# Kernel optimization log

Hardware: AMD Instinct MI355X
Metric: run time of the kernel (lower is better)

The kernel has to match this reference:

```python
import jax, jax.numpy as jnp
from jax import lax
import numpy as np

B, N0 = 4, 4096
NIN, NH, NOUT = 16, 128, 2
DEPTH, K, RADIUS, KNN = 3, 64, 2.0, 3
EPS = 1e-5


def _bn(x, g, b):
    # eval-mode BatchNorm1d with running_mean=0, running_var=1
    return g * x / jnp.sqrt(1.0 + EPS) + b


def _mlp2(h, p):
    # Seq(Lin, ReLU, BN) x 2, as in MLP([d, d, out])
    w1, b1, g1, be1, w2, b2, g2, be2 = p
    h = _bn(jax.nn.relu(h @ w1 + b1), g1, be1)
    return _bn(jax.nn.relu(h @ w2 + b2), g2, be2)


def _fps(pts, m):
    # farthest point sampling, deterministic start at index 0
    n = pts.shape[0]
    def step(carry, _):
        dmin, last = carry
        d = jnp.sum((pts - pts[last]) ** 2, axis=-1)
        dmin = jnp.minimum(dmin, d)
        nxt = jnp.argmax(dmin).astype(jnp.int32)
        return (dmin, nxt), nxt
    _, rest = lax.scan(step, (jnp.full((n,), 1e30, pts.dtype), jnp.int32(0)), None, length=m - 1)
    return jnp.concatenate([jnp.zeros((1,), jnp.int32), rest])


def _sa(xx, pp, m, params):
    # SAModule with PointConv: fps -> radius(K nearest within r) -> gather-MLP-max
    idx = _fps(pp, m)
    q = pp[idx]                                              # [m,3] sampled centers
    d2 = jnp.sum((q[:, None, :] - pp[None, :, :]) ** 2, -1)  # [m,n]
    d2 = jnp.where(d2 <= RADIUS * RADIUS, d2, 1e30)
    neg, nbr = lax.top_k(-d2, K)                             # K nearest inside ball
    valid = neg > -1e29
    h = jnp.concatenate([xx[nbr], pp[nbr] - q[:, None, :]], axis=-1)  # [m,K,C+3]
    h = _mlp2(h, params)
    h = jnp.where(valid[..., None], h, -1e30)
    return jnp.max(h, axis=1), q                             # PointConv max aggr


def _fp(xx, pp, xs, ps, params):
    # FPModule: knn_interpolate (k=3, inverse squared-distance weights) + concat skip + MLP
    d2 = jnp.sum((ps[:, None, :] - pp[None, :, :]) ** 2, -1)  # [n_fine, n_coarse]
    neg, idx = lax.top_k(-d2, KNN)
    w = 1.0 / jnp.maximum(-neg, 1e-16)
    y = jnp.sum(w[..., None] * xx[idx], axis=1) / jnp.sum(w, axis=1, keepdims=True)
    return _mlp2(jnp.concatenate([y, xs], axis=-1), params)


def _forward(x, pos, lin_in_w, lin_in_b,
             sa_w1, sa_b1, sa_g1, sa_be1, sa_w2, sa_b2, sa_g2, sa_be2,
             fp_w1, fp_b1, fp_g1, fp_be1, fp_w2, fp_b2, fp_g2, fp_be2,
             lo_w1, lo_b1, lo_g1, lo_be1, lo_w2, lo_b2, lo_g2, lo_be2):
    xb = jax.nn.relu(x.reshape(B, N0, NIN) @ lin_in_w + lin_in_b)  # lin_in + ReLU
    posb = pos.reshape(B, N0, 3)
    sa = [(xb, posb)]
    n = N0
    for i in range(DEPTH):
        m = n // 2  # ratio = 0.5
        p = (sa_w1[i], sa_b1[i], sa_g1[i], sa_be1[i], sa_w2[i], sa_b2[i], sa_g2[i], sa_be2[i])
        h, q = jax.vmap(lambda a, b: _sa(a, b, m, p))(sa[i][0], sa[i][1])
        sa.append((h, q))
        n = m
    xf, posf = sa[DEPTH]
    for step in range(DEPTH):
        mi = DEPTH - 1 - step
        xs, ps = sa[DEPTH - 1 - step]
        p = (fp_w1[mi], fp_b1[mi], fp_g1[mi], fp_be1[mi], fp_w2[mi], fp_b2[mi], fp_g2[mi], fp_be2[mi])
        xf = jax.vmap(lambda a, b, c, d: _fp(a, b, c, d, p))(xf, posf, xs, ps)
        posf = ps
    out = _mlp2(xf, (lo_w1, lo_b1, lo_g1, lo_be1, lo_w2, lo_b2, lo_g2, lo_be2))
    return out.reshape(B * N0, NOUT)


def setup_inputs() -> dict:
    key = jax.random.key(0)
    ki = iter(jax.random.split(key, 24))
    def nrm(shape, s=0.1):
        return jax.random.normal(next(ki), shape, jnp.float32) * s
    D = NH + 3   # PointConv MLP in-dim
    F = 2 * NH   # FP MLP in-dim (nIn + nSkip)
    return {
        "x": jax.random.normal(next(ki), (B * N0, NIN), jnp.float32),
        "pos": jax.random.uniform(next(ki), (B * N0, 3), jnp.float32) * 16.0,
        "batch": jnp.repeat(jnp.arange(B, dtype=jnp.int32), N0),
        "lin_in_w": nrm((NIN, NH)), "lin_in_b": nrm((NH,)),
        "sa_w1": nrm((DEPTH, D, D)), "sa_b1": nrm((DEPTH, D)),
        "sa_g1": jnp.ones((DEPTH, D)), "sa_be1": jnp.zeros((DEPTH, D)),
        "sa_w2": nrm((DEPTH, D, NH)), "sa_b2": nrm((DEPTH, NH)),
        "sa_g2": jnp.ones((DEPTH, NH)), "sa_be2": jnp.zeros((DEPTH, NH)),
        "fp_w1": nrm((DEPTH, F, F)), "fp_b1": nrm((DEPTH, F)),
        "fp_g1": jnp.ones((DEPTH, F)), "fp_be1": jnp.zeros((DEPTH, F)),
        "fp_w2": nrm((DEPTH, F, NH)), "fp_b2": nrm((DEPTH, NH)),
        "fp_g2": jnp.ones((DEPTH, NH)), "fp_be2": jnp.zeros((DEPTH, NH)),
        "lo_w1": nrm((NH, NH)), "lo_b1": nrm((NH,)),
        "lo_g1": jnp.ones((NH,)), "lo_be1": jnp.zeros((NH,)),
        "lo_w2": nrm((NH, NOUT)), "lo_b2": nrm((NOUT,)),
        "lo_g2": jnp.ones((NOUT,)), "lo_be2": jnp.zeros((NOUT,)),
    }


def reference(x, pos, batch, lin_in_w, lin_in_b,
              sa_w1, sa_b1, sa_g1, sa_be1, sa_w2, sa_b2, sa_g2, sa_be2,
              fp_w1, fp_b1, fp_g1, fp_be1, fp_w2, fp_b2, fp_g2, fp_be2,
              lo_w1, lo_b1, lo_g1, lo_be1, lo_w2, lo_b2, lo_g2, lo_be2):
    return _forward(x, pos, lin_in_w, lin_in_b,
                    sa_w1, sa_b1, sa_g1, sa_be1, sa_w2, sa_b2, sa_g2, sa_be2,
                    fp_w1, fp_b1, fp_g1, fp_be1, fp_w2, fp_b2, fp_g2, fp_be2,
                    lo_w1, lo_b1, lo_g1, lo_be1, lo_w2, lo_b2, lo_g2, lo_be2)
```

## Files before the change

kernel.cpp:

```cpp
#include <hip/hip_runtime.h>
#include <cstddef>


#define EPSF 1e-5f

typedef __attribute__((ext_vector_type(2))) float f32x2;

__device__ __forceinline__ f32x2 f2splat(float s) {
    f32x2 v; v.x = s; v.y = s; return v;
}

__device__ __forceinline__ float d2_rn(float dx, float dy, float dz) {
    return __fadd_rn(__fadd_rn(__fmul_rn(dx, dx), __fmul_rn(dy, dy)), __fmul_rn(dz, dz));
}

template <int CTRL, int RMASK>
__device__ __forceinline__ float dpp_max_f32(float v) {
    int o = __builtin_amdgcn_update_dpp(__float_as_int(v), __float_as_int(v),
                                        CTRL, RMASK, 0xf, false);
    return fmaxf(v, __int_as_float(o));
}

template <int N, int NT>
__device__ void fps_role(const float* __restrict__ pts, float* __restrict__ q,
                         const int m, const int b, char* smem) {
#pragma clang fp contract(off)
    constexpr int PPT = N / NT;
    constexpr int PH = PPT / 2;
    constexpr int NW = NT / 64;
    float* s_px = (float*)smem;
    float* s_py = s_px + N;
    float* s_pz = s_py + N;
    int*   s_qi = (int*)(s_pz + N);
    float2* s_slot = (float2*)(s_qi + N / 2);
    const int t = threadIdx.x;
    const int wave = t >> 6, lane = t & 63;
    const int base = t * PPT;
    const float* P = pts + (size_t)b * N * 3;
    asm volatile("s_setprio 3");
    f32x2 rx[PH], ry[PH], rz[PH], dmin[PH];
#pragma unroll
    for (int j = 0; j < PH; ++j) {
        int i = base + 2 * j;
        float x0 = P[i * 3 + 0], y0 = P[i * 3 + 1], z0 = P[i * 3 + 2];
        float x1 = P[i * 3 + 3], y1 = P[i * 3 + 4], z1 = P[i * 3 + 5];
        rx[j].x = x0; rx[j].y = x1;
        ry[j].x = y0; ry[j].y = y1;
        rz[j].x = z0; rz[j].y = z1;
        dmin[j] = f2splat(1e30f);
        s_px[i] = x0; s_px[i + 1] = x1;
        s_py[i] = y0; s_py[i + 1] = y1;
        s_pz[i] = z0; s_pz[i + 1] = z1;
    }
    float lx = P[0], ly = P[1], lz = P[2];
    if (t == 0) s_qi[0] = 0;

    for (int step = 1; step < m; ++step) {
        float bv = -1.0f; int bj = 0;
        const f32x2 lxv = f2splat(lx), lyv = f2splat(ly), lzv = f2splat(lz);
#pragma unroll
        for (int j = 0; j < PH; ++j) {
            f32x2 dx = rx[j] - lxv;
            f32x2 dy = ry[j] - lyv;
            f32x2 dz = rz[j] - lzv;
            f32x2 d = dx * dx + dy * dy + dz * dz;
            float m0 = fminf(dmin[j].x, d.x);
            float m1 = fminf(dmin[j].y, d.y);
            dmin[j].x = m0; dmin[j].y = m1;
            if (m0 > bv) { bv = m0; bj = 2 * j; }
            if (m1 > bv) { bv = m1; bj = 2 * j + 1; }
        }
        const int bidx = base + bj;

        float v = bv;
        v = dpp_max_f32<0x111, 0xf>(v);
        v = dpp_max_f32<0x112, 0xf>(v);
        v = dpp_max_f32<0x114, 0xf>(v);
        v = dpp_max_f32<0x118, 0xf>(v);
        v = dpp_max_f32<0x142, 0xa>(v);
        v = dpp_max_f32<0x143, 0xc>(v);
        const float mv = __int_as_float(__builtin_amdgcn_readlane(__float_as_int(v), 63));
        unsigned long long mb = __ballot(bv == mv);
        const int wl = __ffsll((long long)mb) - 1;
        const int wbi = __builtin_amdgcn_readlane(bidx, wl);

        const int p = step & 1;
        if (lane == 0) s_slot[p * NW + wave] = make_float2(mv, __int_as_float(wbi));
        __syncthreads();

        float2 sl = s_slot[p * NW + (lane & (NW - 1))];
        float gvt = sl.x;
        gvt = dpp_max_f32<0x111, 0xf>(gvt);
        gvt = dpp_max_f32<0x112, 0xf>(gvt);
        if (NW == 8) gvt = dpp_max_f32<0x114, 0xf>(gvt);
        const float gm = __int_as_float(
            __builtin_amdgcn_readlane(__float_as_int(gvt), NW - 1));
        unsigned long long gb = __ballot((lane < NW) && (sl.x == gm));
        const int gl = __ffsll((long long)gb) - 1;
        const int gi = __builtin_amdgcn_readlane(__float_as_int(sl.y), gl);

        lx = s_px[gi]; ly = s_py[gi]; lz = s_pz[gi];
        if (t == 0) s_qi[step] = gi;
    }
    __syncthreads();
    for (int e = t; e < m; e += NT) {
        int gi = s_qi[e];
        size_t o = ((size_t)b * m + e) * 3;
        q[o] = s_px[gi]; q[o + 1] = s_py[gi]; q[o + 2] = s_pz[gi];
    }
}

__device__ void lin_role(const float* __restrict__ x, const float* __restrict__ w,
                         const float* __restrict__ bias, float* __restrict__ xb,
                         const int blk) {
    const int t = threadIdx.x;
    const int row = blk * 2 + (t >> 7);
    const int col = t & 127;
    float acc = bias[col];
#pragma unroll
    for (int k = 0; k < 16; ++k) acc = fmaf(x[row * 16 + k], w[k * 128 + col], acc);
    xb[row * 128 + col] = fmaxf(acc, 0.0f);
}

template <int CHUNK, int WACT>
__device__ void nbr_role(const float* __restrict__ pts, const float* __restrict__ q,
                         int2* __restrict__ pairs, unsigned* __restrict__ counter,
                         const int n, const int m, const int blk, char* smem) {
    const int w = threadIdx.x >> 6, lane = threadIdx.x & 63;
    if (w >= WACT) return;
    float* D = (float*)smem + w * CHUNK * 64;
    const int c = blk * WACT + w;
    const int b = c / m;
    const float* P = pts + (size_t)b * n * 3;
    const float qx = q[(size_t)c * 3 + 0];
    const float qy = q[(size_t)c * 3 + 1];
    const float qz = q[(size_t)c * 3 + 2];
    for (int s = 0; s < CHUNK; ++s) {
        int i = s * 64 + lane;
        float d2 = d2_rn(P[i * 3] - qx, P[i * 3 + 1] - qy, P[i * 3 + 2] - qz);
        D[i] = (d2 <= 4.0f) ? d2 : 1e30f;
    }
    int my_g = -1;
    int cnt = 0;
    for (int round = 0; round < 64; ++round) {
        float bv = 3e38f;
        int bi = 0x7fffffff;
        for (int s = 0; s < CHUNK; ++s) {
            int i = s * 64 + lane;
            float v = D[i];
            if (v < bv) { bv = v; bi = i; }
        }
#pragma unroll
        for (int off = 32; off >= 1; off >>= 1) {
            float ov = __shfl_xor(bv, off, 64);
            int   oi = __shfl_xor(bi, off, 64);
            if (ov < bv || (ov == bv && oi < bi)) { bv = ov; bi = oi; }
        }
        if (bv > 1e29f) break;
        if (round == lane) my_g = bi;
        if (lane == (bi & 63)) D[bi] = 3e38f;
        ++cnt;
    }
    unsigned base = 0;
    if (lane == 0) base = atomicAdd(counter, (unsigned)cnt);
    base = (unsigned)__shfl((int)base, 0, 64);
    if (lane < cnt) pairs[base + lane] = make_int2(c, my_g);
}

typedef float Row132[132];
__device__ void sa_body(const float* __restrict__ xx, const float* __restrict__ pts,
    const float* __restrict__ q, const int2* __restrict__ pairs,
    const unsigned* __restrict__ vcount,
    const float* __restrict__ wp1, const float* __restrict__ b1,
    const float* __restrict__ g1, const float* __restrict__ be1,
    const float* __restrict__ wp2, const float* __restrict__ b2,
    const float* __restrict__ g2, const float* __restrict__ be2,
    float* __restrict__ hout, const int lm, const int ln, const int blk, char* smem) {
    Row132* shA = (Row132*)smem;
    int* sh_c = (int*)(smem + 33792);
    int* sh_g = sh_c + 64;
    const int t = threadIdx.x;
    const int V = (int)*vcount;
    const int r0 = blk * 64;
    if (r0 >= V) return;
    if (t < 64) {
        int r = r0 + t;
        if (r < V) { int2 p = pairs[r]; sh_c[t] = p.x; sh_g[t] = p.y; }
        else { sh_c[t] = -1; sh_g[t] = 0; }
    }
    __syncthreads();

    for (int e = t; e < 64 * 33; e += 256) {
        int row = e / 33, cid = e - row * 33;
        int c = sh_c[row];
        float4 v = make_float4(0.f, 0.f, 0.f, 0.f);
        if (c >= 0) {
            int g = sh_g[row];
            int b = c >> lm;
            size_t pt = ((size_t)(b << ln) + g);
            if (cid < 32) {
                v = *(const float4*)(xx + (pt << 7) + cid * 4);
            } else {
                const float* P = pts + pt * 3;
                const float* Q = q + (size_t)c * 3;
                v.x = P[0] - Q[0]; v.y = P[1] - Q[1]; v.z = P[2] - Q[2]; v.w = 0.f;
            }
        }
        *(float4*)&shA[row][cid * 4] = v;
    }
    __syncthreads();

    const float invs = 1.0f / sqrtf(1.0f + EPSF);
    const int tr = t >> 4, tc = t & 15;
    const int xrow = t >> 2, xcol = t & 3;
    float acc[32];
#pragma unroll
    for (int i = 0; i < 32; ++i) acc[i] = 0.0f;
    float accx = 0.0f;

    for (int k = 0; k < 132; k += 4) {
        const float4 A0 = *(const float4*)&shA[tr     ][k];
        const float4 A1 = *(const float4*)&shA[tr + 16][k];
        const float4 A2 = *(const float4*)&shA[tr + 32][k];
        const float4 A3 = *(const float4*)&shA[tr + 48][k];
        const float4 AX = *(const float4*)&shA[xrow][k];
        const float a0v[4] = {A0.x, A0.y, A0.z, A0.w};
        const float a1v[4] = {A1.x, A1.y, A1.z, A1.w};
        const float a2v[4] = {A2.x, A2.y, A2.z, A2.w};
        const float a3v[4] = {A3.x, A3.y, A3.z, A3.w};
        const float axv[4] = {AX.x, AX.y, AX.z, AX.w};
#pragma unroll
        for (int u = 0; u < 4; ++u) {
            const float* wr = wp1 + (size_t)(k + u) * 132;
            const float4 w0 = *(const float4*)(wr + 8 * tc);
            const float4 w1v = *(const float4*)(wr + 8 * tc + 4);
            const float wx = wr[128 + xcol];
            const float wa[8] = {w0.x, w0.y, w0.z, w0.w, w1v.x, w1v.y, w1v.z, w1v.w};
#pragma unroll
            for (int j = 0; j < 8; ++j) {
                acc[0 * 8 + j] = fmaf(a0v[u], wa[j], acc[0 * 8 + j]);
                acc[1 * 8 + j] = fmaf(a1v[u], wa[j], acc[1 * 8 + j]);
                acc[2 * 8 + j] = fmaf(a2v[u], wa[j], acc[2 * 8 + j]);
                acc[3 * 8 + j] = fmaf(a3v[u], wa[j], acc[3 * 8 + j]);
            }
            accx = fmaf(axv[u], wx, accx);
        }
    }
    __syncthreads();
#pragma unroll
    for (int i = 0; i < 4; ++i)
#pragma unroll
        for (int j = 0; j < 8; ++j) {
            int col = 8 * tc + j;
            float z = fmaxf(acc[i * 8 + j] + b1[col], 0.0f);
            shA[tr + 16 * i][col] = g1[col] * z * invs + be1[col];
        }
    if (xcol < 3) {
        int col = 128 + xcol;
        float z = fmaxf(accx + b1[col], 0.0f);
        shA[xrow][col] = g1[col] * z * invs + be1[col];
    } else {
        shA[xrow][131] = 0.0f;
    }
    __syncthreads();

#pragma unroll
    for (int i = 0; i < 32; ++i) acc[i] = 0.0f;
    for (int k = 0; k < 132; k += 4) {
        const float4 A0 = *(const float4*)&shA[tr     ][k];
        const float4 A1 = *(const float4*)&shA[tr + 16][k];
        const float4 A2 = *(const float4*)&shA[tr + 32][k];
        const float4 A3 = *(const float4*)&shA[tr + 48][k];
        const float a0v[4] = {A0.x, A0.y, A0.z, A0.w};
        const float a1v[4] = {A1.x, A1.y, A1.z, A1.w};
        const float a2v[4] = {A2.x, A2.y, A2.z, A2.w};
        const float a3v[4] = {A3.x, A3.y, A3.z, A3.w};
#pragma unroll
        for (int u = 0; u < 4; ++u) {
            const float* wr = wp2 + (size_t)(k + u) * 128;
            const float4 w0 = *(const float4*)(wr + 8 * tc);
            const float4 w1v = *(const float4*)(wr + 8 * tc + 4);
            const float wa[8] = {w0.x, w0.y, w0.z, w0.w, w1v.x, w1v.y, w1v.z, w1v.w};
#pragma unroll
            for (int j = 0; j < 8; ++j) {
                acc[0 * 8 + j] = fmaf(a0v[u], wa[j], acc[0 * 8 + j]);
                acc[1 * 8 + j] = fmaf(a1v[u], wa[j], acc[1 * 8 + j]);
                acc[2 * 8 + j] = fmaf(a2v[u], wa[j], acc[2 * 8 + j]);
                acc[3 * 8 + j] = fmaf(a3v[u], wa[j], acc[3 * 8 + j]);
            }
        }
    }
    __syncthreads();
#pragma unroll
    for (int i = 0; i < 4; ++i)
#pragma unroll
        for (int j = 0; j < 8; ++j) {
            int col = 8 * tc + j;
            float z = fmaxf(acc[i * 8 + j] + b2[col], 0.0f);
            shA[tr + 16 * i][col] = g2[col] * z * invs + be2[col];
        }
    __syncthreads();

    if (t < 128) {
        const int col = t;
        float run = -1.0f;
        int cur = sh_c[0];
        for (int row = 0; row < 64; ++row) {
            int c = sh_c[row];
            if (c != cur) {
                if (cur >= 0)
                    atomicMax((unsigned*)&hout[((size_t)cur << 7) + col], __float_as_uint(run));
                run = -1.0f; cur = c;
            }
            run = fmaxf(run, shA[row][col]);
        }
        if (cur >= 0)
            atomicMax((unsigned*)&hout[((size_t)cur << 7) + col], __float_as_uint(run));
    }
}

__device__ void knn_role(const float* __restrict__ pf, const float* __restrict__ pc,
                         int* __restrict__ kidx, float* __restrict__ kw,
                         const int nf, const int nc, const int blk) {
    const int tg = blk * 256 + threadIdx.x;
    const int b = tg / nf;
    const float* F = pf + (size_t)tg * 3;
    const float fx = F[0], fy = F[1], fz = F[2];
    const float* C = pc + (size_t)b * nc * 3;
    float b0 = 1e30f, b1 = 1e30f, b2 = 1e30f;
    int i0 = 0, i1 = 0, i2 = 0;
    for (int j = 0; j < nc; ++j) {
        float d2 = d2_rn(C[j * 3] - fx, C[j * 3 + 1] - fy, C[j * 3 + 2] - fz);
        if (d2 < b0)      { b2 = b1; i2 = i1; b1 = b0; i1 = i0; b0 = d2; i0 = j; }
        else if (d2 < b1) { b2 = b1; i2 = i1; b1 = d2; i1 = j; }
        else if (d2 < b2) { b2 = d2; i2 = j; }
    }
    float w0 = 1.0f / fmaxf(b0, 1e-16f);
    float w1 = 1.0f / fmaxf(b1, 1e-16f);
    float w2 = 1.0f / fmaxf(b2, 1e-16f);
    float inv = 1.0f / (w0 + w1 + w2);
    size_t o = (size_t)tg * 3;
    kidx[o] = i0; kidx[o + 1] = i1; kidx[o + 2] = i2;
    kw[o] = w0 * inv; kw[o + 1] = w1 * inv; kw[o + 2] = w2 * inv;
}

__global__ __launch_bounds__(256) void stage_a_kernel(
    const float* __restrict__ pos, float* __restrict__ q1,
    const float* __restrict__ x, const float* __restrict__ lin_w,
    const float* __restrict__ lin_b, float* __restrict__ xb,
    float* __restrict__ hbuf, unsigned* __restrict__ ctrs,
    const float* __restrict__ sa_w1, const float* __restrict__ sa_w2,
    float* __restrict__ wp1, float* __restrict__ wp2) {
    __shared__ __align__(16) char smem[57408];
    const int blk = blockIdx.x;
    if (blk < 4) {
        fps_role<4096, 256>(pos, q1, 2048, blk, smem);
    } else if (blk < 4 + 8192) {
        lin_role(x, lin_w, lin_b, xb, blk - 4);
    } else if (blk < 4 + 8192 + 1792) {
        const int i = blk - 8196;
        *(float4*)(hbuf + (size_t)i * 1024 + threadIdx.x * 4) =
            make_float4(0.f, 0.f, 0.f, 0.f);
        if (i == 0 && threadIdx.x < 3) ctrs[threadIdx.x * 16] = 0u;
    } else {
        const int f = (blk - 9988) * 256 + threadIdx.x;
        if (f < 52272) {
            int col = f % 132; int r = f / 132;
            int k = r % 132; int lvl = r / 132;
            float v = 0.0f;
            if (k < 131 && col < 131)
                v = sa_w1[(size_t)lvl * 131 * 131 + k * 131 + col];
            wp1[f] = v;
        } else if (f < 52272 + 50688) {
            int f2 = f - 52272;
            int col = f2 & 127; int r = f2 >> 7;
            int k = r % 132; int lvl = r / 132;
            float v = 0.0f;
            if (k < 131)
                v = sa_w2[(size_t)lvl * 131 * 128 + k * 128 + col];
            wp2[f2] = v;
        }
    }
}

__global__ __launch_bounds__(256) void stage_b_kernel(
    const float* __restrict__ q1, float* __restrict__ q2,
    const float* __restrict__ pos, int2* __restrict__ pairs1,
    unsigned* __restrict__ ctr0,
    int* __restrict__ kidx2, float* __restrict__ kw2) {
    __shared__ __align__(16) char smem[32768];
    const int blk = blockIdx.x;
    if (blk < 4) fps_role<2048, 256>(q1, q2, 1024, blk, smem);
    else if (blk < 4 + 4096)
        nbr_role<64, 2>(pos, q1, pairs1, ctr0, 4096, 2048, blk - 4, smem);
    else
        knn_role(pos, q1, kidx2, kw2, 4096, 2048, blk - 4100);
}

__global__ __launch_bounds__(256) void stage_c_kernel(
    const float* __restrict__ q2, float* __restrict__ q3,
    const float* __restrict__ q1, int2* __restrict__ pairs2,
    unsigned* __restrict__ ctr1,
    const float* __restrict__ xb, const float* __restrict__ pos,
    const int2* __restrict__ pairs1, const unsigned* __restrict__ ctr0,
    const float* __restrict__ wp1, const float* __restrict__ b1,
    const float* __restrict__ g1, const float* __restrict__ be1,
    const float* __restrict__ wp2, const float* __restrict__ b2,
    const float* __restrict__ g2, const float* __restrict__ be2,
    float* __restrict__ h1, int* __restrict__ kidx1, float* __restrict__ kw1) {
    __shared__ __align__(16) char smem[34304];
    const int blk = blockIdx.x;
    if (blk < 4) fps_role<1024, 256>(q2, q3, 512, blk, smem);
    else if (blk < 4 + 1024)
        nbr_role<32, 4>(q1, q2, pairs2, ctr1, 2048, 1024, blk - 4, smem);
    else if (blk < 4 + 1024 + 8192)
        sa_body(xb, pos, q1, pairs1, ctr0, wp1, b1, g1, be1, wp2, b2, g2, be2,
                h1, 11, 12, blk - 1028, smem);
    else
        knn_role(q1, q2, kidx1, kw1, 2048, 1024, blk - 9220);
}

__global__ __launch_bounds__(256) void stage_d_kernel(
    const float* __restrict__ q2, const float* __restrict__ q3,
    int2* __restrict__ pairs3, unsigned* __restrict__ ctr2,
    const float* __restrict__ h1, const float* __restrict__ q1,
    const int2* __restrict__ pairs2, const unsigned* __restrict__ ctr1,
    const float* __restrict__ wp1, const float* __restrict__ b1,
    const float* __restrict__ g1, const float* __restrict__ be1,
    const float* __restrict__ wp2, const float* __restrict__ b2,
    const float* __restrict__ g2, const float* __restrict__ be2,
    float* __restrict__ h2, int* __restrict__ kidx0, float* __restrict__ kw0) {
    __shared__ __align__(16) char smem[34304];
    const int blk = blockIdx.x;
    if (blk < 512) nbr_role<16, 4>(q2, q3, pairs3, ctr2, 1024, 512, blk, smem);
    else if (blk < 512 + 16) knn_role(q2, q3, kidx0, kw0, 1024, 512, blk - 512);
    else
        sa_body(h1, q1, q2, pairs2, ctr1, wp1, b1, g1, be1, wp2, b2, g2, be2,
                h2, 10, 11, blk - 528, smem);
}

__global__ __launch_bounds__(256) void sa_fused_kernel(
    const float* xx, const float* pts, const float* q, const int2* pairs,
    const unsigned* vcount,
    const float* wp1, const float* b1, const float* g1, const float* be1,
    const float* wp2, const float* b2, const float* g2, const float* be2,
    float* hout, int lm, int ln) {
    __shared__ __align__(16) char smem[34304];
    sa_body(xx, pts, q, pairs, vcount, wp1, b1, g1, be1, wp2, b2, g2, be2,
            hout, lm, ln, blockIdx.x, smem);
}

__global__ __launch_bounds__(256) void fp_fused_kernel(
    const float* __restrict__ xc, const float* __restrict__ xs,
    const int* __restrict__ kidx, const float* __restrict__ kw,
    const float* __restrict__ w1, const float* __restrict__ b1,
    const float* __restrict__ g1, const float* __restrict__ be1,
    const float* __restrict__ w2, const float* __restrict__ b2,
    const float* __restrict__ g2, const float* __restrict__ be2,
    float* __restrict__ out, int lnf) {
    __shared__ __align__(16) float shA[32][260];
    const int t = threadIdx.x;
    const int r0 = blockIdx.x * 32;
    const float invs = 1.0f / sqrtf(1.0f + EPSF);

    for (int e = t; e < 32 * 64; e += 256) {
        int r = e >> 6, cid = e & 63;
        int fr = r0 + r;
        float4 v;
        if (cid < 32) {
            int b = fr >> lnf;
            size_t o = (size_t)fr * 3;
            int i0 = kidx[o], i1 = kidx[o + 1], i2 = kidx[o + 2];
            float u0 = kw[o], u1 = kw[o + 1], u2 = kw[o + 2];
            const float* X = xc + (((size_t)b << lnf) >> 1) * 128;
            const float4 A0 = *(const float4*)(X + (size_t)i0 * 128 + cid * 4);
            const float4 A1 = *(const float4*)(X + (size_t)i1 * 128 + cid * 4);
            const float4 A2 = *(const float4*)(X + (size_t)i2 * 128 + cid * 4);
            v.x = u0 * A0.x + u1 * A1.x + u2 * A2.x;
            v.y = u0 * A0.y + u1 * A1.y + u2 * A2.y;
            v.z = u0 * A0.z + u1 * A1.z + u2 * A2.z;
            v.w = u0 * A0.w + u1 * A1.w + u2 * A2.w;
        } else {
            v = *(const float4*)(xs + (size_t)fr * 128 + (cid - 32) * 4);
        }
        *(float4*)&shA[r][cid * 4] = v;
    }
    __syncthreads();

    const int tr = t >> 5, tc = t & 31;
    float acc[32];
#pragma unroll
    for (int i = 0; i < 32; ++i) acc[i] = 0.0f;
    for (int k = 0; k < 256; k += 4) {
        const float4 A0 = *(const float4*)&shA[tr     ][k];
        const float4 A1 = *(const float4*)&shA[tr +  8][k];
        const float4 A2 = *(const float4*)&shA[tr + 16][k];
        const float4 A3 = *(const float4*)&shA[tr + 24][k];
        const float a0v[4] = {A0.x, A0.y, A0.z, A0.w};
        const float a1v[4] = {A1.x, A1.y, A1.z, A1.w};
        const float a2v[4] = {A2.x, A2.y, A2.z, A2.w};
        const float a3v[4] = {A3.x, A3.y, A3.z, A3.w};
#pragma unroll
        for (int u = 0; u < 4; ++u) {
            const float* wr = w1 + (size_t)(k + u) * 256;
            const float4 w0v = *(const float4*)(wr + 8 * tc);
            const float4 w1v = *(const float4*)(wr + 8 * tc + 4);
            const float wa[8] = {w0v.x, w0v.y, w0v.z, w0v.w, w1v.x, w1v.y, w1v.z, w1v.w};
#pragma unroll
            for (int j = 0; j < 8; ++j) {
                acc[0 * 8 + j] = fmaf(a0v[u], wa[j], acc[0 * 8 + j]);
                acc[1 * 8 + j] = fmaf(a1v[u], wa[j], acc[1 * 8 + j]);
                acc[2 * 8 + j] = fmaf(a2v[u], wa[j], acc[2 * 8 + j]);
                acc[3 * 8 + j] = fmaf(a3v[u], wa[j], acc[3 * 8 + j]);
            }
        }
    }
    __syncthreads();
#pragma unroll
    for (int i = 0; i < 4; ++i)
#pragma unroll
        for (int j = 0; j < 8; ++j) {
            int col = 8 * tc + j;
            float z = fmaxf(acc[i * 8 + j] + b1[col], 0.0f);
            shA[tr + 8 * i][col] = g1[col] * z * invs + be1[col];
        }
    __syncthreads();

    const int tr2 = t >> 4, tc2 = t & 15;
    float acc2[16];
#pragma unroll
    for (int i = 0; i < 16; ++i) acc2[i] = 0.0f;
    for (int k = 0; k < 256; k += 4) {
        const float4 A0 = *(const float4*)&shA[tr2     ][k];
        const float4 A1 = *(const float4*)&shA[tr2 + 16][k];
        const float a0v[4] = {A0.x, A0.y, A0.z, A0.w};
        const float a1v[4] = {A1.x, A1.y, A1.z, A1.w};
#pragma unroll
        for (int u = 0; u < 4; ++u) {
            const float* wr = w2 + (size_t)(k + u) * 128;
            const float4 w0v = *(const float4*)(wr + 8 * tc2);
            const float4 w1v = *(const float4*)(wr + 8 * tc2 + 4);
            const float wa[8] = {w0v.x, w0v.y, w0v.z, w0v.w, w1v.x, w1v.y, w1v.z, w1v.w};
#pragma unroll
            for (int j = 0; j < 8; ++j) {
                acc2[0 * 8 + j] = fmaf(a0v[u], wa[j], acc2[0 * 8 + j]);
                acc2[1 * 8 + j] = fmaf(a1v[u], wa[j], acc2[1 * 8 + j]);
            }
        }
    }
#pragma unroll
    for (int i = 0; i < 2; ++i)
#pragma unroll
        for (int j = 0; j < 8; ++j) {
            int col = 8 * tc2 + j;
            int fr = r0 + tr2 + 16 * i;
            float z = fmaxf(acc2[i * 8 + j] + b2[col], 0.0f);
            out[(size_t)fr * 128 + col] = g2[col] * z * invs + be2[col];
        }
}

__global__ __launch_bounds__(256) void lo_fused_kernel(
    const float* __restrict__ in,
    const float* __restrict__ w1, const float* __restrict__ b1,
    const float* __restrict__ g1, const float* __restrict__ be1,
    const float* __restrict__ w2, const float* __restrict__ b2,
    const float* __restrict__ g2, const float* __restrict__ be2,
    float* __restrict__ out) {
    __shared__ __align__(16) float shA[32][132];
    const int t = threadIdx.x;
    const int r0 = blockIdx.x * 32;
    const float invs = 1.0f / sqrtf(1.0f + EPSF);

    for (int e = t; e < 32 * 32; e += 256) {
        int r = e >> 5, cid = e & 31;
        *(float4*)&shA[r][cid * 4] =
            *(const float4*)(in + (size_t)(r0 + r) * 128 + cid * 4);
    }
    __syncthreads();

    const int tr = t >> 4, tc = t & 15;
    float acc[16];
#pragma unroll
    for (int i = 0; i < 16; ++i) acc[i] = 0.0f;
    for (int k = 0; k < 128; k += 4) {
        const float4 A0 = *(const float4*)&shA[2 * tr + 0][k];
        const float4 A1 = *(const float4*)&shA[2 * tr + 1][k];
        const float a0v[4] = {A0.x, A0.y, A0.z, A0.w};
        const float a1v[4] = {A1.x, A1.y, A1.z, A1.w};
#pragma unroll
        for (int u = 0; u < 4; ++u) {
            const float* wr = w1 + (size_t)(k + u) * 128;
            const float4 w0v = *(const float4*)(wr + 8 * tc);
            const float4 w1v = *(const float4*)(wr + 8 * tc + 4);
            const float wa[8] = {w0v.x, w0v.y, w0v.z, w0v.w, w1v.x, w1v.y, w1v.z, w1v.w};
#pragma unroll
            for (int j = 0; j < 8; ++j) {
                acc[0 * 8 + j] = fmaf(a0v[u], wa[j], acc[0 * 8 + j]);
                acc[1 * 8 + j] = fmaf(a1v[u], wa[j], acc[1 * 8 + j]);
            }
        }
    }
    __syncthreads();
#pragma unroll
    for (int i = 0; i < 2; ++i)
#pragma unroll
        for (int j = 0; j < 8; ++j) {
            int col = 8 * tc + j;
            float z = fmaxf(acc[i * 8 + j] + b1[col], 0.0f);
            shA[2 * tr + i][col] = g1[col] * z * invs + be1[col];
        }
    __syncthreads();

    if (t < 64) {
        const int row = t >> 1, col = t & 1;
        float a = b2[col];
        for (int k = 0; k < 128; ++k)
            a = fmaf(shA[row][k], w2[k * 2 + col], a);
        a = fmaxf(a, 0.0f);
        out[(size_t)(r0 + row) * 2 + col] = g2[col] * a * invs + be2[col];
    }
}

extern "C" void kernel_launch(void* const* d_in, const int* in_sizes, int n_in,
                              void* d_out, int out_size, void* d_ws, size_t ws_size,
                              hipStream_t stream) {
    const float* x      = (const float*)d_in[0];
    const float* pos    = (const float*)d_in[1];
    const float* lin_w  = (const float*)d_in[3];
    const float* lin_b  = (const float*)d_in[4];
    const float* sa_w1  = (const float*)d_in[5];
    const float* sa_b1  = (const float*)d_in[6];
    const float* sa_g1  = (const float*)d_in[7];
    const float* sa_be1 = (const float*)d_in[8];
    const float* sa_w2  = (const float*)d_in[9];
    const float* sa_b2  = (const float*)d_in[10];
    const float* sa_g2  = (const float*)d_in[11];
    const float* sa_be2 = (const float*)d_in[12];
    const float* fp_w1  = (const float*)d_in[13];
    const float* fp_b1  = (const float*)d_in[14];
    const float* fp_g1  = (const float*)d_in[15];
    const float* fp_be1 = (const float*)d_in[16];
    const float* fp_w2  = (const float*)d_in[17];
    const float* fp_b2  = (const float*)d_in[18];
    const float* fp_g2  = (const float*)d_in[19];
    const float* fp_be2 = (const float*)d_in[20];
    const float* lo_w1  = (const float*)d_in[21];
    const float* lo_b1  = (const float*)d_in[22];
    const float* lo_g1  = (const float*)d_in[23];
    const float* lo_be1 = (const float*)d_in[24];
    const float* lo_w2  = (const float*)d_in[25];
    const float* lo_b2  = (const float*)d_in[26];
    const float* lo_g2  = (const float*)d_in[27];
    const float* lo_be2 = (const float*)d_in[28];

    float* ws = (float*)d_ws;
    size_t off = 0;
    auto alloc = [&](size_t n) { float* p = ws + off; off += n; return p; };
    float* xb    = alloc(4 * 4096 * 128);
    float* q1    = alloc(4 * 2048 * 3);
    float* q2    = alloc(4 * 1024 * 3);
    float* q3    = alloc(4 * 512 * 3);
    float* h1    = alloc(4 * 2048 * 128);
    float* h2    = alloc(4 * 1024 * 128);
    float* h3    = alloc(4 * 512 * 128);
    int2* pairs1 = (int2*)alloc(4 * 2048 * 64 * 2);
    int2* pairs2 = (int2*)alloc(4 * 1024 * 64 * 2);
    int2* pairs3 = (int2*)alloc(4 * 512 * 64 * 2);
    unsigned* ctrs = (unsigned*)alloc(64);
    int* kidx0   = (int*)alloc(4 * 1024 * 3);
    float* kw0   = alloc(4 * 1024 * 3);
    int* kidx1   = (int*)alloc(4 * 2048 * 3);
    float* kw1   = alloc(4 * 2048 * 3);
    int* kidx2   = (int*)alloc(4 * 4096 * 3);
    float* kw2   = alloc(4 * 4096 * 3);
    float* xfA   = alloc(4 * 4096 * 128);
    float* xfB   = alloc(4 * 4096 * 128);
    float* wp1   = alloc(3 * 132 * 132);
    float* wp2   = alloc(3 * 132 * 128);
    if (ws_size < off * sizeof(float)) return;

    stage_a_kernel<<<4 + 8192 + 1792 + 403, 256, 0, stream>>>(
        pos, q1, x, lin_w, lin_b, xb, h1, ctrs, sa_w1, sa_w2, wp1, wp2);

    stage_b_kernel<<<4 + 4096 + 64, 256, 0, stream>>>(
        q1, q2, pos, pairs1, ctrs + 0, kidx2, kw2);

    stage_c_kernel<<<4 + 1024 + 8192 + 32, 256, 0, stream>>>(
        q2, q3, q1, pairs2, ctrs + 16,
        xb, pos, pairs1, ctrs + 0,
        wp1, sa_b1, sa_g1, sa_be1, wp2, sa_b2, sa_g2, sa_be2, h1,
        kidx1, kw1);

    stage_d_kernel<<<512 + 16 + 4096, 256, 0, stream>>>(
        q2, q3, pairs3, ctrs + 32,
        h1, q1, pairs2, ctrs + 16,
        wp1 + 132 * 132, sa_b1 + 131, sa_g1 + 131, sa_be1 + 131,
        wp2 + 132 * 128, sa_b2 + 128, sa_g2 + 128, sa_be2 + 128, h2,
        kidx0, kw0);

    sa_fused_kernel<<<2048, 256, 0, stream>>>(h2, q2, q3, pairs3, ctrs + 32,
        wp1 + 2 * 132 * 132, sa_b1 + 2 * 131, sa_g1 + 2 * 131, sa_be1 + 2 * 131,
        wp2 + 2 * 132 * 128, sa_b2 + 2 * 128, sa_g2 + 2 * 128, sa_be2 + 2 * 128,
        h3, 9, 10);

    fp_fused_kernel<<<4 * 1024 / 32, 256, 0, stream>>>(h3, h2, kidx0, kw0,
        fp_w1 + 2 * 256 * 256, fp_b1 + 2 * 256, fp_g1 + 2 * 256, fp_be1 + 2 * 256,
        fp_w2 + 2 * 256 * 128, fp_b2 + 2 * 128, fp_g2 + 2 * 128, fp_be2 + 2 * 128,
        xfA, 10);

    fp_fused_kernel<<<4 * 2048 / 32, 256, 0, stream>>>(xfA, h1, kidx1, kw1,
        fp_w1 + 256 * 256, fp_b1 + 256, fp_g1 + 256, fp_be1 + 256,
        fp_w2 + 256 * 128, fp_b2 + 128, fp_g2 + 128, fp_be2 + 128,
        xfB, 11);

    fp_fused_kernel<<<4 * 4096 / 32, 256, 0, stream>>>(xfB, xb, kidx2, kw2,
        fp_w1, fp_b1, fp_g1, fp_be1, fp_w2, fp_b2, fp_g2, fp_be2,
        xfA, 12);

    lo_fused_kernel<<<16384 / 32, 256, 0, stream>>>(xfA,
        lo_w1, lo_b1, lo_g1, lo_be1, lo_w2, lo_b2, lo_g2, lo_be2,
        (float*)d_out);
}
```

Baseline: 3.089 ms.

## Reuse first-level FPS prefix as deeper sample sets and merge neighbor searches

Farthest point sampling started at index 0 is nested: re-sampling an FPS-ordered set yields its own prefix. So the second and third FPS passes are dropped and q2/q3 become prefixes of q1, addressed through new stride parameters. All radius-neighbor and kNN searches for the three levels now run in one stage_b launch. The three SA levels then run as separate sa_fused launches instead of overlapping with FPS roles. This removes two long serial FPS passes, at the cost of possible tie-breaking differences from the reference argmax order.

```diff
diff --git a/kernel.cpp b/kernel.cpp
--- a/kernel.cpp
+++ b/kernel.cpp
@@ -125,16 +125,19 @@
 template <int CHUNK, int WACT>
 __device__ void nbr_role(const float* __restrict__ pts, const float* __restrict__ q,
                          int2* __restrict__ pairs, unsigned* __restrict__ counter,
-                         const int n, const int m, const int blk, char* smem) {
+                         const int n, const int m, const int pstr, const int qstr,
+                         const int blk, char* smem) {
     const int w = threadIdx.x >> 6, lane = threadIdx.x & 63;
     if (w >= WACT) return;
     float* D = (float*)smem + w * CHUNK * 64;
     const int c = blk * WACT + w;
     const int b = c / m;
-    const float* P = pts + (size_t)b * n * 3;
-    const float qx = q[(size_t)c * 3 + 0];
-    const float qy = q[(size_t)c * 3 + 1];
-    const float qz = q[(size_t)c * 3 + 2];
+    const int r = c - b * m;
+    const float* P = pts + (size_t)b * pstr * 3;
+    const size_t qo = ((size_t)b * qstr + r) * 3;
+    const float qx = q[qo + 0];
+    const float qy = q[qo + 1];
+    const float qz = q[qo + 2];
     for (int s = 0; s < CHUNK; ++s) {
         int i = s * 64 + lane;
         float d2 = d2_rn(P[i * 3] - qx, P[i * 3 + 1] - qy, P[i * 3 + 2] - qz);
@@ -168,14 +171,15 @@
 }
 
 typedef float Row132[132];
-__device__ void sa_body(const float* __restrict__ xx, const float* __restrict__ pts,
-    const float* __restrict__ q, const int2* __restrict__ pairs,
+__device__ void sa_body(const float* __restrict__ xx, const float* __restrict__ ptsc,
+    const float* __restrict__ qc, const int2* __restrict__ pairs,
     const unsigned* __restrict__ vcount,
     const float* __restrict__ wp1, const float* __restrict__ b1,
     const float* __restrict__ g1, const float* __restrict__ be1,
     const float* __restrict__ wp2, const float* __restrict__ b2,
     const float* __restrict__ g2, const float* __restrict__ be2,
-    float* __restrict__ hout, const int lm, const int ln, const int blk, char* smem) {
+    float* __restrict__ hout, const int lm, const int ln, const int lnp,
+    const int blk, char* smem) {
     Row132* shA = (Row132*)smem;
     int* sh_c = (int*)(smem + 33792);
     int* sh_g = sh_c + 64;
@@ -197,12 +201,14 @@
         if (c >= 0) {
             int g = sh_g[row];
             int b = c >> lm;
-            size_t pt = ((size_t)(b << ln) + g);
             if (cid < 32) {
-                v = *(const float4*)(xx + (pt << 7) + cid * 4);
+                size_t ptf = ((size_t)(b << ln) + g);
+                v = *(const float4*)(xx + (ptf << 7) + cid * 4);
             } else {
-                const float* P = pts + pt * 3;
-                const float* Q = q + (size_t)c * 3;
+                size_t ptc = ((size_t)(b << lnp) + g);
+                const float* P = ptsc + ptc * 3;
+                int r = c - (b << lm);
+                const float* Q = qc + ((size_t)((b << 11) + r)) * 3;
                 v.x = P[0] - Q[0]; v.y = P[1] - Q[1]; v.z = P[2] - Q[2]; v.w = 0.f;
             }
         }
@@ -321,12 +327,14 @@
 
 __device__ void knn_role(const float* __restrict__ pf, const float* __restrict__ pc,
                          int* __restrict__ kidx, float* __restrict__ kw,
-                         const int nf, const int nc, const int blk) {
+                         const int nf, const int nc, const int fstr, const int cstr,
+                         const int blk) {
     const int tg = blk * 256 + threadIdx.x;
     const int b = tg / nf;
-    const float* F = pf + (size_t)tg * 3;
+    const int rf = tg - b * nf;
+    const float* F = pf + ((size_t)b * fstr + rf) * 3;
     const float fx = F[0], fy = F[1], fz = F[2];
-    const float* C = pc + (size_t)b * nc * 3;
+    const float* C = pc + (size_t)b * cstr * 3;
     float b0 = 1e30f, b1 = 1e30f, b2 = 1e30f;
     int i0 = 0, i1 = 0, i2 = 0;
     for (int j = 0; j < nc; ++j) {
@@ -384,70 +392,38 @@
 }
 
 __global__ __launch_bounds__(256) void stage_b_kernel(
-    const float* __restrict__ q1, float* __restrict__ q2,
-    const float* __restrict__ pos, int2* __restrict__ pairs1,
-    unsigned* __restrict__ ctr0,
-    int* __restrict__ kidx2, float* __restrict__ kw2) {
+    const float* __restrict__ pos, const float* __restrict__ q1,
+    int2* __restrict__ pairs1, unsigned* __restrict__ ctr0,
+    int2* __restrict__ pairs2, unsigned* __restrict__ ctr1,
+    int2* __restrict__ pairs3, unsigned* __restrict__ ctr2,
+    int* __restrict__ kidx2, float* __restrict__ kw2,
+    int* __restrict__ kidx1, float* __restrict__ kw1,
+    int* __restrict__ kidx0, float* __restrict__ kw0) {
     __shared__ __align__(16) char smem[32768];
     const int blk = blockIdx.x;
-    if (blk < 4) fps_role<2048, 256>(q1, q2, 1024, blk, smem);
-    else if (blk < 4 + 4096)
-        nbr_role<64, 2>(pos, q1, pairs1, ctr0, 4096, 2048, blk - 4, smem);
+    if (blk < 4096)
+        nbr_role<64, 2>(pos, q1, pairs1, ctr0, 4096, 2048, 4096, 2048, blk, smem);
+    else if (blk < 4096 + 1024)
+        nbr_role<32, 4>(q1, q1, pairs2, ctr1, 2048, 1024, 2048, 2048, blk - 4096, smem);
+    else if (blk < 4096 + 1024 + 512)
+        nbr_role<16, 4>(q1, q1, pairs3, ctr2, 1024, 512, 2048, 2048, blk - 5120, smem);
+    else if (blk < 5632 + 64)
+        knn_role(pos, q1, kidx2, kw2, 4096, 2048, 4096, 2048, blk - 5632);
+    else if (blk < 5696 + 32)
+        knn_role(q1, q1, kidx1, kw1, 2048, 1024, 2048, 2048, blk - 5696);
     else
-        knn_role(pos, q1, kidx2, kw2, 4096, 2048, blk - 4100);
-}
-
-__global__ __launch_bounds__(256) void stage_c_kernel(
-    const float* __restrict__ q2, float* __restrict__ q3,
-    const float* __restrict__ q1, int2* __restrict__ pairs2,
-    unsigned* __restrict__ ctr1,
-    const float* __restrict__ xb, const float* __restrict__ pos,
-    const int2* __restrict__ pairs1, const unsigned* __restrict__ ctr0,
-    const float* __restrict__ wp1, const float* __restrict__ b1,
-    const float* __restrict__ g1, const float* __restrict__ be1,
-    const float* __restrict__ wp2, const float* __restrict__ b2,
-    const float* __restrict__ g2, const float* __restrict__ be2,
-    float* __restrict__ h1, int* __restrict__ kidx1, float* __restrict__ kw1) {
-    __shared__ __align__(16) char smem[34304];
-    const int blk = blockIdx.x;
-    if (blk < 4) fps_role<1024, 256>(q2, q3, 512, blk, smem);
-    else if (blk < 4 + 1024)
-        nbr_role<32, 4>(q1, q2, pairs2, ctr1, 2048, 1024, blk - 4, smem);
-    else if (blk < 4 + 1024 + 8192)
-        sa_body(xb, pos, q1, pairs1, ctr0, wp1, b1, g1, be1, wp2, b2, g2, be2,
-                h1, 11, 12, blk - 1028, smem);
-    else
-        knn_role(q1, q2, kidx1, kw1, 2048, 1024, blk - 9220);
-}
-
-__global__ __launch_bounds__(256) void stage_d_kernel(
-    const float* __restrict__ q2, const float* __restrict__ q3,
-    int2* __restrict__ pairs3, unsigned* __restrict__ ctr2,
-    const float* __restrict__ h1, const float* __restrict__ q1,
-    const int2* __restrict__ pairs2, const unsigned* __restrict__ ctr1,
-    const float* __restrict__ wp1, const float* __restrict__ b1,
-    const float* __restrict__ g1, const float* __restrict__ be1,
-    const float* __restrict__ wp2, const float* __restrict__ b2,
-    const float* __restrict__ g2, const float* __restrict__ be2,
-    float* __restrict__ h2, int* __restrict__ kidx0, float* __restrict__ kw0) {
-    __shared__ __align__(16) char smem[34304];
-    const int blk = blockIdx.x;
-    if (blk < 512) nbr_role<16, 4>(q2, q3, pairs3, ctr2, 1024, 512, blk, smem);
-    else if (blk < 512 + 16) knn_role(q2, q3, kidx0, kw0, 1024, 512, blk - 512);
-    else
-        sa_body(h1, q1, q2, pairs2, ctr1, wp1, b1, g1, be1, wp2, b2, g2, be2,
-                h2, 10, 11, blk - 528, smem);
+        knn_role(q1, q1, kidx0, kw0, 1024, 512, 2048, 2048, blk - 5728);
 }
 
 __global__ __launch_bounds__(256) void sa_fused_kernel(
-    const float* xx, const float* pts, const float* q, const int2* pairs,
+    const float* xx, const float* ptsc, const float* qc, const int2* pairs,
     const unsigned* vcount,
     const float* wp1, const float* b1, const float* g1, const float* be1,
     const float* wp2, const float* b2, const float* g2, const float* be2,
-    float* hout, int lm, int ln) {
+    float* hout, int lm, int ln, int lnp) {
     __shared__ __align__(16) char smem[34304];
-    sa_body(xx, pts, q, pairs, vcount, wp1, b1, g1, be1, wp2, b2, g2, be2,
-            hout, lm, ln, blockIdx.x, smem);
+    sa_body(xx, ptsc, qc, pairs, vcount, wp1, b1, g1, be1, wp2, b2, g2, be2,
+            hout, lm, ln, lnp, blockIdx.x, smem);
 }
 
 __global__ __launch_bounds__(256) void fp_fused_kernel(
@@ -658,8 +634,6 @@
     auto alloc = [&](size_t n) { float* p = ws + off; off += n; return p; };
     float* xb    = alloc(4 * 4096 * 128);
     float* q1    = alloc(4 * 2048 * 3);
-    float* q2    = alloc(4 * 1024 * 3);
-    float* q3    = alloc(4 * 512 * 3);
     float* h1    = alloc(4 * 2048 * 128);
     float* h2    = alloc(4 * 1024 * 128);
     float* h3    = alloc(4 * 512 * 128);
@@ -682,26 +656,23 @@
     stage_a_kernel<<<4 + 8192 + 1792 + 403, 256, 0, stream>>>(
         pos, q1, x, lin_w, lin_b, xb, h1, ctrs, sa_w1, sa_w2, wp1, wp2);
 
-    stage_b_kernel<<<4 + 4096 + 64, 256, 0, stream>>>(
-        q1, q2, pos, pairs1, ctrs + 0, kidx2, kw2);
-
-    stage_c_kernel<<<4 + 1024 + 8192 + 32, 256, 0, stream>>>(
-        q2, q3, q1, pairs2, ctrs + 16,
-        xb, pos, pairs1, ctrs + 0,
-        wp1, sa_b1, sa_g1, sa_be1, wp2, sa_b2, sa_g2, sa_be2, h1,
-        kidx1, kw1);
-
-    stage_d_kernel<<<512 + 16 + 4096, 256, 0, stream>>>(
-        q2, q3, pairs3, ctrs + 32,
-        h1, q1, pairs2, ctrs + 16,
+    stage_b_kernel<<<4096 + 1024 + 512 + 64 + 32 + 16, 256, 0, stream>>>(
+        pos, q1, pairs1, ctrs + 0, pairs2, ctrs + 16, pairs3, ctrs + 32,
+        kidx2, kw2, kidx1, kw1, kidx0, kw0);
+
+    sa_fused_kernel<<<8192, 256, 0, stream>>>(xb, pos, q1, pairs1, ctrs + 0,
+        wp1, sa_b1, sa_g1, sa_be1, wp2, sa_b2, sa_g2, sa_be2,
+        h1, 11, 12, 12);
+
+    sa_fused_kernel<<<4096, 256, 0, stream>>>(h1, q1, q1, pairs2, ctrs + 16,
         wp1 + 132 * 132, sa_b1 + 131, sa_g1 + 131, sa_be1 + 131,
-        wp2 + 132 * 128, sa_b2 + 128, sa_g2 + 128, sa_be2 + 128, h2,
-        kidx0, kw0);
-
-    sa_fused_kernel<<<2048, 256, 0, stream>>>(h2, q2, q3, pairs3, ctrs + 32,
+        wp2 + 132 * 128, sa_b2 + 128, sa_g2 + 128, sa_be2 + 128,
+        h2, 10, 11, 11);
+
+    sa_fused_kernel<<<2048, 256, 0, stream>>>(h2, q1, q1, pairs3, ctrs + 32,
         wp1 + 2 * 132 * 132, sa_b1 + 2 * 131, sa_g1 + 2 * 131, sa_be1 + 2 * 131,
         wp2 + 2 * 132 * 128, sa_b2 + 2 * 128, sa_g2 + 2 * 128, sa_be2 + 2 * 128,
-        h3, 9, 10);
+        h3, 9, 10, 11);
 
     fp_fused_kernel<<<4 * 1024 / 32, 256, 0, stream>>>(h3, h2, kidx0, kw0,
         fp_w1 + 2 * 256 * 256, fp_b1 + 2 * 256, fp_g1 + 2 * 256, fp_be1 + 2 * 256,
```

Result: faster. 2.699 ms (median of 2 runs) (-12.6%).
